# Performance work log

Hardware: AMD Instinct MI355X
Metric: run time of the kernel (lower is better)

Reference implementation:

```python
import jax, jax.numpy as jnp
import numpy as np

N_EMBED = 2048
N_HEAD = 16
HEAD_DIM = N_EMBED // N_HEAD
LN_EPS = 1e-5


def setup_inputs() -> dict:
    key = jax.random.key(0)
    ks = jax.random.split(key, 12)
    B, S, D = 4, 2048, N_EMBED
    s = 0.02
    inp = {
        "x": jax.random.normal(ks[0], (B, S, D), jnp.float32),
        "ln1_w": jnp.ones((D,), jnp.float32),
        "ln1_b": jnp.zeros((D,), jnp.float32),
        "Wqkv": jax.random.normal(ks[1], (3 * D, D), jnp.float32) * s,
        "bqkv": jnp.zeros((3 * D,), jnp.float32),
        "Wo": jax.random.normal(ks[2], (D, D), jnp.float32) * s,
        "bo": jnp.zeros((D,), jnp.float32),
        "ln2_w": jnp.ones((D,), jnp.float32),
        "ln2_b": jnp.zeros((D,), jnp.float32),
        "W1": jax.random.normal(ks[3], (4 * D, D), jnp.float32) * s,
        "b1": jnp.zeros((4 * D,), jnp.float32),
        "W2": jax.random.normal(ks[4], (D, 4 * D), jnp.float32) * s,
        "b2": jnp.zeros((D,), jnp.float32),
        # ALiBi slopes: 2^(-8*(h+1)/n_head)
        "slopes": jnp.asarray(2.0 ** (-8.0 * (np.arange(1, N_HEAD + 1)) / N_HEAD), jnp.float32),
    }
    return inp


def layer_norm(x, w, b):
    mu = jnp.mean(x, axis=-1, keepdims=True)
    var = jnp.mean(jnp.square(x - mu), axis=-1, keepdims=True)
    return (x - mu) * jax.lax.rsqrt(var + LN_EPS) * w + b


def attention(h, Wqkv, bqkv, Wo, bo, slopes):
    B, S, D = h.shape
    qkv = jnp.einsum("bsd,ed->bse", h, Wqkv) + bqkv  # [B,S,3D]
    q, k, v = jnp.split(qkv, 3, axis=-1)
    q = q.reshape(B, S, N_HEAD, HEAD_DIM).transpose(0, 2, 1, 3)
    k = k.reshape(B, S, N_HEAD, HEAD_DIM).transpose(0, 2, 1, 3)
    v = v.reshape(B, S, N_HEAD, HEAD_DIM).transpose(0, 2, 1, 3)
    scores = jnp.einsum("bhqd,bhkd->bhqk", q, k) / jnp.sqrt(jnp.float32(HEAD_DIM))
    pos = jnp.arange(S)
    rel = pos[None, :] - pos[:, None]  # j - i, <= 0 on causal part
    alibi = slopes[:, None, None] * rel[None, :, :].astype(jnp.float32)  # [H,S,S]
    causal = rel <= 0
    scores = jnp.where(causal[None, None], scores + alibi[None], -jnp.inf)
    attn = jax.nn.softmax(scores, axis=-1)
    out = jnp.einsum("bhqk,bhkd->bhqd", attn, v)
    out = out.transpose(0, 2, 1, 3).reshape(B, S, D)
    return jnp.einsum("bsd,ed->bse", out, Wo) + bo


def reference(x, ln1_w, ln1_b, Wqkv, bqkv, Wo, bo, ln2_w, ln2_b, W1, b1, W2, b2, slopes):
    # Pre-LN block; dropout in eval mode (identity)
    x = x + attention(layer_norm(x, ln1_w, ln1_b), Wqkv, bqkv, Wo, bo, slopes)
    h = layer_norm(x, ln2_w, ln2_b)
    h = jax.nn.gelu(jnp.einsum("bsd,fd->bsf", h, W1) + b1, approximate=False)
    x = x + jnp.einsum("bsf,df->bsd", h, W2) + b2
    return x
```

## Files before the change

### kernel.cpp

```cpp
#include <hip/hip_runtime.h>

typedef unsigned short ushort_t;
typedef __attribute__((ext_vector_type(8))) short short8;
typedef __attribute__((ext_vector_type(4))) float floatx4;
typedef __attribute__((ext_vector_type(4))) unsigned short ush4;

#define MFMA16x16x32(a, b, c) __builtin_amdgcn_mfma_f32_16x16x32_bf16(a, b, c, 0, 0, 0)

__device__ __forceinline__ float bf2f(ushort_t h) {
    unsigned int u = ((unsigned int)h) << 16;
    return __builtin_bit_cast(float, u);
}
__device__ __forceinline__ ushort_t f2bf(float f) {
    unsigned int u = __builtin_bit_cast(unsigned int, f);
    u += 0x7fffu + ((u >> 16) & 1u);
    return (ushort_t)(u >> 16);
}
__device__ __forceinline__ void gload_lds16(const ushort_t* g, ushort_t* l) {
    __builtin_amdgcn_global_load_lds(
        (const __attribute__((address_space(1))) unsigned int*)g,
        (__attribute__((address_space(3))) unsigned int*)l, 16, 0, 0);
}

__global__ __launch_bounds__(256) void conv_bf16(const float* __restrict__ in,
                                                 ushort_t* __restrict__ out, int n8) {
    int i = blockIdx.x * 256 + threadIdx.x;
    const int stride = gridDim.x * 256;
    for (; i < n8; i += stride) {
        const float* p = in + (size_t)i * 8;
        floatx4 a0 = *(const floatx4*)p;
        floatx4 a1 = *(const floatx4*)(p + 4);
        short8 o;
        o[0] = (short)f2bf(a0[0]); o[1] = (short)f2bf(a0[1]);
        o[2] = (short)f2bf(a0[2]); o[3] = (short)f2bf(a0[3]);
        o[4] = (short)f2bf(a1[0]); o[5] = (short)f2bf(a1[1]);
        o[6] = (short)f2bf(a1[2]); o[7] = (short)f2bf(a1[3]);
        *(short8*)(out + (size_t)i * 8) = o;
    }
}

template <int INF32>
__global__ __launch_bounds__(256) void ln_kernel(const void* __restrict__ in,
                                                 const ushort_t* __restrict__ w,
                                                 const ushort_t* __restrict__ b,
                                                 ushort_t* __restrict__ out) {
    const int row = blockIdx.x;
    const int tid = threadIdx.x;
    const size_t base = (size_t)row * 2048 + (size_t)tid * 8;
    float v[8];
    if (INF32) {
        const float* p = (const float*)in + base;
        floatx4 a0 = *(const floatx4*)p;
        floatx4 a1 = *(const floatx4*)(p + 4);
        v[0] = a0[0]; v[1] = a0[1]; v[2] = a0[2]; v[3] = a0[3];
        v[4] = a1[0]; v[5] = a1[1]; v[6] = a1[2]; v[7] = a1[3];
    } else {
        short8 hv = *(const short8*)((const ushort_t*)in + base);
        const ushort_t* hp = (const ushort_t*)&hv;
#pragma unroll
        for (int k = 0; k < 8; k++) v[k] = bf2f(hp[k]);
    }
    float s = 0.f, sq = 0.f;
#pragma unroll
    for (int k = 0; k < 8; k++) { s += v[k]; sq += v[k] * v[k]; }
#pragma unroll
    for (int m = 32; m; m >>= 1) { s += __shfl_xor(s, m); sq += __shfl_xor(sq, m); }
    __shared__ float red[8];
    const int wv = tid >> 6;
    if ((tid & 63) == 0) { red[wv] = s; red[4 + wv] = sq; }
    __syncthreads();
    s = red[0] + red[1] + red[2] + red[3];
    sq = red[4] + red[5] + red[6] + red[7];
    const float mu = s * (1.f / 2048.f);
    const float var = fmaxf(sq * (1.f / 2048.f) - mu * mu, 0.f);
    const float rs = rsqrtf(var + 1e-5f);
    short8 ov;
#pragma unroll
    for (int k = 0; k < 8; k++) {
        const int c = tid * 8 + k;
        float y = (v[k] - mu) * rs * bf2f(w[c]) + bf2f(b[c]);
        ov[k] = (short)f2bf(y);
    }
    *(short8*)(out + base) = ov;
}

template <int EPI>
__global__ __launch_bounds__(512, 2) void gemm256(const ushort_t* __restrict__ A,
                                                  const ushort_t* __restrict__ W,
                                                  const ushort_t* __restrict__ bias,
                                                  const void* __restrict__ res,
                                                  void* __restrict__ out,
                                                  int M, int N, int K) {
    __shared__ ushort_t smem[65536];
    const int tid = threadIdx.x;
    const int lane = tid & 63;
    const int wave = tid >> 6;
    const int la = lane & 15;
    const int qd = lane >> 4;
    const int wrow = (wave >> 2) * 128;
    const int wcol = (wave & 3) * 64;
    const int nbn = N >> 8;
    int bm, bn;
    {
        int wg = (int)blockIdx.x;
        const int cpx = (int)gridDim.x >> 3;
        wg = (wg & 7) * cpx + (wg >> 3);
        const int per = 8 * nbn;
        const int g = wg / per;
        const int rem = wg - g * per;
        bm = g * 8 + (rem & 7);
        bn = rem >> 3;
    }
    const int srow = tid >> 2;
    const int schunk = (tid & 3) ^ ((srow >> 1) & 3);
    const ushort_t* gA = A + (size_t)(bm * 256 + srow) * K + schunk * 8;
    const ushort_t* gB = W + (size_t)(bn * 256 + srow) * K + schunk * 8;
    const int wbase = (tid & ~63) * 8;
    const int kch = (qd ^ ((la >> 1) & 3)) * 8;

    floatx4 acc[8][4];
    const floatx4 z4 = {0.f, 0.f, 0.f, 0.f};
#pragma unroll
    for (int i = 0; i < 8; i++)
#pragma unroll
        for (int j = 0; j < 4; j++) acc[i][j] = z4;
    short8 a[8], b[4];

#define GBAR() __builtin_amdgcn_s_barrier()
#define GVM8() asm volatile("s_waitcnt vmcnt(8)")
#define STGA(koff, b_)                                                                  \
    do {                                                                                \
        gload_lds16(gA + (size_t)(koff), smem + (b_)*16384 + wbase);                    \
        gload_lds16(gA + (size_t)128 * K + (size_t)(koff),                              \
                    smem + (b_)*16384 + 4096 + wbase);                                  \
    } while (0)
#define STGB(koff, b_)                                                                  \
    do {                                                                                \
        gload_lds16(gB + (size_t)(koff), smem + (b_)*16384 + 8192 + wbase);             \
        gload_lds16(gB + (size_t)128 * K + (size_t)(koff),                              \
                    smem + (b_)*16384 + 12288 + wbase);                                 \
    } while (0)
#define LDAF(b_, mh)                                                                    \
    do {                                                                                \
        _Pragma("unroll") for (int mi = 0; mi < 4; mi++) {                              \
            a[(mh)*4 + mi] = *(const short8*)&smem[(b_)*16384 +                         \
                                          (wrow + (mh)*64 + mi * 16 + la) * 32 + kch];  \
        }                                                                               \
    } while (0)
#define LDBF(b_)                                                                        \
    do {                                                                                \
        _Pragma("unroll") for (int nj = 0; nj < 4; nj++) {                              \
            b[nj] = *(const short8*)&smem[(b_)*16384 + 8192 +                           \
                                          (wcol + nj * 16 + la) * 32 + kch];            \
        }                                                                               \
    } while (0)
#define MM32()                                                                          \
    do {                                                                                \
        _Pragma("unroll") for (int mi = 0; mi < 8; mi++)                                \
            _Pragma("unroll") for (int nj = 0; nj < 4; nj++) acc[mi][nj] =              \
                MFMA16x16x32(a[mi], b[nj], acc[mi][nj]);                                \
    } while (0)
#define KITER(u)                                                                        \
    do {                                                                                \
        GVM8();                                                                         \
        GBAR();                                                                         \
        const int pre_ = (t + (u) + 3 < NT) ? (t + (u) + 3) : (NT - 1);                 \
        const size_t ko_ = (size_t)pre_ * 32;                                           \
        STGA(ko_, ((u) + 3) & 3);                                                       \
        STGB(ko_, ((u) + 3) & 3);                                                       \
        LDAF((u), 0); LDBF((u)); LDAF((u), 1);                                          \
        __builtin_amdgcn_s_setprio(1); MM32(); __builtin_amdgcn_s_setprio(0);           \
    } while (0)

    const int NT = K >> 5;
    STGA(0, 0); STGB(0, 0);
    STGA(32, 1); STGB(32, 1);
    STGA(64, 2); STGB(64, 2);

    for (int t = 0; t < NT; t += 4) { KITER(0); KITER(1); KITER(2); KITER(3); }
    asm volatile("s_waitcnt vmcnt(0)");
    GBAR();
#undef GBAR
#undef GVM8
#undef STGA
#undef STGB
#undef LDAF
#undef LDBF
#undef MM32
#undef KITER

    if (EPI == 0) {
        ushort_t* q_out = (ushort_t*)out;
        if (bn < 16) {
            const float qs = (bn < 8) ? (0.08838834764831845f * 1.4426950408889634f) : 1.0f;
            ushort_t* dst = (bn < 8) ? q_out : (q_out + 16777216);
#pragma unroll
            for (int i = 0; i < 8; i++)
#pragma unroll
                for (int j = 0; j < 4; j++)
#pragma unroll
                    for (int r = 0; r < 4; r++) {
                        const int m = bm * 256 + wrow + i * 16 + qd * 4 + r;
                        const int n = bn * 256 + wcol + j * 16 + la;
                        dst[(size_t)m * 2048 + (n & 2047)] =
                            f2bf((acc[i][j][r] + bf2f(bias[n])) * qs);
                    }
        } else {
            ushort_t* v_out = q_out + 33554432;
#pragma unroll
            for (int i = 0; i < 8; i++)
#pragma unroll
                for (int j = 0; j < 4; j++) {
                    const int n = bn * 256 + wcol + j * 16 + la;
                    const int d = n - 4096;
                    const int m0 = bm * 256 + wrow + i * 16 + qd * 4;
                    const int bb = m0 >> 11, s = m0 & 2047;
                    const float bv = bf2f(bias[n]);
                    ush4 pk;
#pragma unroll
                    for (int r = 0; r < 4; r++) pk[r] = f2bf(acc[i][j][r] + bv);
                    *(ush4*)&v_out[((size_t)(bb * 2048 + d)) * 2048 + s] = pk;
                }
        }
    } else {
#pragma unroll
        for (int i = 0; i < 8; i++)
#pragma unroll
            for (int j = 0; j < 4; j++)
#pragma unroll
                for (int r = 0; r < 4; r++) {
                    const int m = bm * 256 + wrow + i * 16 + qd * 4 + r;
                    const int n = bn * 256 + wcol + j * 16 + la;
                    const size_t idx = (size_t)m * N + n;
                    float v = acc[i][j][r] + bf2f(bias[n]);
                    if (EPI == 1) {
                        v += ((const float*)res)[idx];
                        ((ushort_t*)out)[idx] = f2bf(v);
                    } else if (EPI == 2) {
                        v = 0.5f * v * (1.f + erff(v * 0.70710678118654752f));
                        ((ushort_t*)out)[idx] = f2bf(v);
                    } else {
                        v += bf2f(((const ushort_t*)res)[idx]);
                        ((float*)out)[idx] = v;
                    }
                }
    }
}

__global__ __launch_bounds__(256, 2) void attn_kernel(const ushort_t* __restrict__ qb,
                                                      const ushort_t* __restrict__ kb,
                                                      const ushort_t* __restrict__ vtb,
                                                      const float* __restrict__ slopes,
                                                      ushort_t* __restrict__ out) {
    __shared__ ushort_t Ks[16384];
    __shared__ ushort_t Vt[16384];
    __shared__ ushort_t Ps[4096];
    const int tid = threadIdx.x;
    const int lane = tid & 63;
    const int wave = tid >> 6;
    const int la = lane & 15;
    const int qd = lane >> 4;
    const int lid = (int)blockIdx.x;
    const int pair = (lid & 7) * 8 + (lid >> 8);
    const int h = pair & 15;
    const int b = pair >> 4;
    const int qt = 31 - ((lid >> 3) & 31);
    const float slope2 = slopes[h] * 1.4426950408889634f;

    const size_t qrow = (size_t)(b * 2048 + qt * 64 + wave * 16 + la);
    short8 qa[4];
#pragma unroll
    for (int ks = 0; ks < 4; ks++)
        qa[ks] = *(const short8*)&qb[qrow * 2048 + h * 128 + (ks * 4 + qd) * 8];

    const ushort_t* kbase = kb + ((size_t)b * 2048) * 2048 + h * 128;
    const ushort_t* vbase = vtb + ((size_t)(b * 2048 + h * 128)) * 2048;

    floatx4 accO[8];
    const floatx4 z4 = {0.f, 0.f, 0.f, 0.f};
#pragma unroll
    for (int dt = 0; dt < 8; dt++) accO[dt] = z4;
    float mst[4] = {-1e30f, -1e30f, -1e30f, -1e30f};
    float lst[4] = {0.f, 0.f, 0.f, 0.f};

#define AISSUE(kt_, buf_)                                                                   \
    do {                                                                                    \
        _Pragma("unroll") for (int p_ = 0; p_ < 4; p_++) {                                  \
            const int f_ = p_ * 256 + tid;                                                  \
            const int r_ = f_ >> 4;                                                         \
            const int cs_ = f_ & 15;                                                        \
            gload_lds16(kbase + (size_t)((kt_) * 64 + r_) * 2048 + (cs_ ^ (r_ & 15)) * 8,   \
                        Ks + (buf_) * 8192 + (size_t)(p_ * 256 + (tid & ~63)) * 8);         \
        }                                                                                   \
        _Pragma("unroll") for (int p_ = 0; p_ < 4; p_++) {                                  \
            const int f_ = p_ * 256 + tid;                                                  \
            const int d_ = f_ >> 3;                                                         \
            const int c_ = f_ & 7;                                                          \
            gload_lds16(vbase + (size_t)d_ * 2048 + (kt_) * 64 + (c_ ^ (d_ & 7)) * 8,       \
                        Vt + (buf_) * 8192 + (size_t)(p_ * 256 + (tid & ~63)) * 8);         \
        }                                                                                   \
    } while (0)
#define ABAR() __builtin_amdgcn_s_barrier()

    AISSUE(0, 0);
    for (int kt = 0; kt <= qt; kt++) {
        const int cur = kt & 1;
        if (kt < qt) {
            AISSUE(kt + 1, cur ^ 1);
            asm volatile("s_waitcnt vmcnt(8)");
        } else {
            asm volatile("s_waitcnt vmcnt(0)");
        }
        ABAR();
        const ushort_t* Kc = Ks + cur * 8192;
        const ushort_t* Vc = Vt + cur * 8192;

        floatx4 sc[4];
#pragma unroll
        for (int nt = 0; nt < 4; nt++) sc[nt] = z4;
#pragma unroll
        for (int nt = 0; nt < 4; nt++) {
#pragma unroll
            for (int ks = 0; ks < 4; ks++) {
                short8 kf = *(const short8*)&Kc[(nt * 16 + la) * 128 + ((ks * 4 + qd) ^ la) * 8];
                sc[nt] = MFMA16x16x32(qa[ks], kf, sc[nt]);
            }
        }

        const int knb = kt * 64;
        const bool diag = (kt == qt);
        ushort_t* Pw = Ps + wave * 1024;
        float acol[4];
#pragma unroll
        for (int nt = 0; nt < 4; nt++)
            acol[nt] = slope2 * (float)(knb + nt * 16 + la);
#pragma unroll
        for (int r = 0; r < 4; r++) {
            float rmax = -1e30f;
#pragma unroll
            for (int nt = 0; nt < 4; nt++) {
                float sval = sc[nt][r] + acol[nt];
                if (diag && (nt * 16 + la > wave * 16 + qd * 4 + r)) sval = -1e30f;
                sc[nt][r] = sval;
                rmax = fmaxf(rmax, sval);
            }
            rmax = fmaxf(rmax, __shfl_xor(rmax, 1));
            rmax = fmaxf(rmax, __shfl_xor(rmax, 2));
            rmax = fmaxf(rmax, __shfl_xor(rmax, 4));
            rmax = fmaxf(rmax, __shfl_xor(rmax, 8));
            const float mnew = fmaxf(mst[r], rmax);
            const int row = qd * 4 + r;
            float rsum = 0.f;
#pragma unroll
            for (int nt = 0; nt < 4; nt++) {
                const float pv = __builtin_amdgcn_exp2f(sc[nt][r] - mnew);
                rsum += pv;
                const int col = nt * 16 + la;
                Pw[row * 64 + ((col >> 3) ^ (row & 7)) * 8 + (col & 7)] = f2bf(pv);
            }
            rsum += __shfl_xor(rsum, 1);
            rsum += __shfl_xor(rsum, 2);
            rsum += __shfl_xor(rsum, 4);
            rsum += __shfl_xor(rsum, 8);
            const float alpha = __builtin_amdgcn_exp2f(mst[r] - mnew);
            mst[r] = mnew;
            lst[r] = lst[r] * alpha + rsum;
#pragma unroll
            for (int dt = 0; dt < 8; dt++) accO[dt][r] *= alpha;
        }

#pragma unroll
        for (int k2 = 0; k2 < 2; k2++) {
            short8 pa = *(const short8*)&Pw[la * 64 + ((k2 * 4 + qd) ^ (la & 7)) * 8];
#pragma unroll
            for (int dt = 0; dt < 8; dt++) {
                const int d = dt * 16 + la;
                short8 vf = *(const short8*)&Vc[d * 64 + ((k2 * 4 + qd) ^ (d & 7)) * 8];
                accO[dt] = MFMA16x16x32(pa, vf, accO[dt]);
            }
        }
        ABAR();
    }
#undef AISSUE
#undef ABAR

    const size_t orow0 = (size_t)b * 2048 + qt * 64 + wave * 16 + qd * 4;
#pragma unroll
    for (int r = 0; r < 4; r++) {
        const float inv = 1.f / lst[r];
#pragma unroll
        for (int dt = 0; dt < 8; dt++)
            out[(orow0 + r) * 2048 + h * 128 + dt * 16 + la] = f2bf(accO[dt][r] * inv);
    }
}

extern "C" void kernel_launch(void* const* d_in, const int* in_sizes, int n_in,
                              void* d_out, int out_size, void* d_ws, size_t ws_size,
                              hipStream_t stream) {
    (void)in_sizes; (void)n_in; (void)out_size; (void)ws_size;
    const float* x      = (const float*)d_in[0];
    const float* ln1w   = (const float*)d_in[1];
    const float* ln1b   = (const float*)d_in[2];
    const float* Wqkv   = (const float*)d_in[3];
    const float* bqkv   = (const float*)d_in[4];
    const float* Wo     = (const float*)d_in[5];
    const float* bo     = (const float*)d_in[6];
    const float* ln2w   = (const float*)d_in[7];
    const float* ln2b   = (const float*)d_in[8];
    const float* W1     = (const float*)d_in[9];
    const float* b1     = (const float*)d_in[10];
    const float* W2     = (const float*)d_in[11];
    const float* b2     = (const float*)d_in[12];
    const float* slopes = (const float*)d_in[13];
    float* outp = (float*)d_out;

    char* ws = (char*)d_ws;
    const size_t MB = 1ull << 20;
    ushort_t* wbuf  = (ushort_t*)(ws);
    ushort_t* sv    = (ushort_t*)(ws + 36 * MB);
    ushort_t* ln1w_c = sv;
    ushort_t* ln1b_c = sv + 2048;
    ushort_t* bqkv_c = sv + 4096;
    ushort_t* bo_c   = sv + 10240;
    ushort_t* ln2w_c = sv + 12288;
    ushort_t* ln2b_c = sv + 14336;
    ushort_t* b1_c   = sv + 16384;
    ushort_t* b2_c   = sv + 24576;
    ushort_t* h_buf    = (ushort_t*)(ws + 37 * MB);
    ushort_t* q_buf    = (ushort_t*)(ws + 69 * MB);
    ushort_t* k_buf    = (ushort_t*)(ws + 101 * MB);
    ushort_t* vt_buf   = (ushort_t*)(ws + 133 * MB);
    ushort_t* attn_buf = (ushort_t*)(ws + 165 * MB);
    ushort_t* act_buf  = q_buf;
    ushort_t* x2_buf   = (ushort_t*)(ws + 197 * MB);

    const int M = 8192;

    conv_bf16<<<8, 256, 0, stream>>>(ln1w, ln1w_c, 2048 / 8);
    conv_bf16<<<8, 256, 0, stream>>>(ln1b, ln1b_c, 2048 / 8);
    ln_kernel<1><<<M, 256, 0, stream>>>(x, ln1w_c, ln1b_c, h_buf);
    conv_bf16<<<2048, 256, 0, stream>>>(Wqkv, wbuf, (6144 * 2048) / 8);
    conv_bf16<<<8, 256, 0, stream>>>(bqkv, bqkv_c, 6144 / 8);
    gemm256<0><<<(M / 256) * (6144 / 256), 512, 0, stream>>>(
        h_buf, wbuf, bqkv_c, nullptr, q_buf, M, 6144, 2048);
    attn_kernel<<<2048, 256, 0, stream>>>(q_buf, k_buf, vt_buf, slopes, attn_buf);
    conv_bf16<<<1024, 256, 0, stream>>>(Wo, wbuf, (2048 * 2048) / 8);
    conv_bf16<<<8, 256, 0, stream>>>(bo, bo_c, 2048 / 8);
    gemm256<1><<<(M / 256) * (2048 / 256), 512, 0, stream>>>(
        attn_buf, wbuf, bo_c, x, x2_buf, M, 2048, 2048);
    conv_bf16<<<8, 256, 0, stream>>>(ln2w, ln2w_c, 2048 / 8);
    conv_bf16<<<8, 256, 0, stream>>>(ln2b, ln2b_c, 2048 / 8);
    ln_kernel<0><<<M, 256, 0, stream>>>(x2_buf, ln2w_c, ln2b_c, h_buf);
    conv_bf16<<<2048, 256, 0, stream>>>(W1, wbuf, (8192 * 2048) / 8);
    conv_bf16<<<8, 256, 0, stream>>>(b1, b1_c, 8192 / 8);
    gemm256<2><<<(M / 256) * (8192 / 256), 512, 0, stream>>>(
        h_buf, wbuf, b1_c, nullptr, act_buf, M, 8192, 2048);
    conv_bf16<<<2048, 256, 0, stream>>>(W2, wbuf, (2048 * 8192) / 8);
    conv_bf16<<<8, 256, 0, stream>>>(b2, b2_c, 2048 / 8);
    gemm256<3><<<(M / 256) * (2048 / 256), 512, 0, stream>>>(
        act_buf, wbuf, b2_c, x2_buf, outp, M, 2048, 8192);
}
```

Before: 1.270 ms.

## Double-buffer GEMM LDS fragments in registers to overlap loads with MFMA

The bf16 GEMM main loop now keeps two register sets of A/B fragments. It reads the next k-tile from LDS right after the barrier, then issues the global prefetch, then runs the MFMAs on the current tile. Base pointers per LDS stage are precomputed, and a sched_barrier keeps the compiler from moving the loads back into the MFMA block. The wait count and prologue change to match: an extra wait and barrier before the first fragment load. This hides LDS read latency behind matrix math, at the cost of roughly 64 more VGPRs for the second fragment set and a tighter synchronisation ordering.

```diff
diff --git a/kernel.cpp b/kernel.cpp
--- a/kernel.cpp
+++ b/kernel.cpp
@@ -117,6 +117,13 @@
     const ushort_t* gB = W + (size_t)(bn * 256 + srow) * K + schunk * 8;
     const int wbase = (tid & ~63) * 8;
     const int kch = (qd ^ ((la >> 1) & 3)) * 8;
+    const ushort_t* aB[4];
+    const ushort_t* bB[4];
+#pragma unroll
+    for (int q = 0; q < 4; q++) {
+        aB[q] = smem + q * 16384 + (wrow + la) * 32 + kch;
+        bB[q] = smem + q * 16384 + 8192 + (wcol + la) * 32 + kch;
+    }
 
     floatx4 acc[8][4];
     const floatx4 z4 = {0.f, 0.f, 0.f, 0.f};
@@ -124,10 +131,10 @@
     for (int i = 0; i < 8; i++)
 #pragma unroll
         for (int j = 0; j < 4; j++) acc[i][j] = z4;
-    short8 a[8], b[4];
+    short8 a[2][8], b[2][4];
 
 #define GBAR() __builtin_amdgcn_s_barrier()
-#define GVM8() asm volatile("s_waitcnt vmcnt(8)")
+#define GVM4() asm volatile("s_waitcnt vmcnt(4)")
 #define STGA(koff, b_)                                                                  \
     do {                                                                                \
         gload_lds16(gA + (size_t)(koff), smem + (b_)*16384 + wbase);                    \
@@ -140,52 +147,50 @@
         gload_lds16(gB + (size_t)128 * K + (size_t)(koff),                              \
                     smem + (b_)*16384 + 12288 + wbase);                                 \
     } while (0)
-#define LDAF(b_, mh)                                                                    \
+#define LDF(buf_, s_)                                                                   \
     do {                                                                                \
-        _Pragma("unroll") for (int mi = 0; mi < 4; mi++) {                              \
-            a[(mh)*4 + mi] = *(const short8*)&smem[(b_)*16384 +                         \
-                                          (wrow + (mh)*64 + mi * 16 + la) * 32 + kch];  \
-        }                                                                               \
-    } while (0)
-#define LDBF(b_)                                                                        \
-    do {                                                                                \
-        _Pragma("unroll") for (int nj = 0; nj < 4; nj++) {                              \
-            b[nj] = *(const short8*)&smem[(b_)*16384 + 8192 +                           \
-                                          (wcol + nj * 16 + la) * 32 + kch];            \
-        }                                                                               \
-    } while (0)
-#define MM32()                                                                          \
+        _Pragma("unroll") for (int mi = 0; mi < 4; mi++)                                \
+            a[s_][mi] = *(const short8*)(aB[buf_] + mi * 512);                          \
+        _Pragma("unroll") for (int nj = 0; nj < 4; nj++)                                \
+            b[s_][nj] = *(const short8*)(bB[buf_] + nj * 512);                          \
+        _Pragma("unroll") for (int mi = 0; mi < 4; mi++)                                \
+            a[s_][4 + mi] = *(const short8*)(aB[buf_] + 2048 + mi * 512);               \
+    } while (0)
+#define MM32(s_)                                                                        \
     do {                                                                                \
         _Pragma("unroll") for (int mi = 0; mi < 8; mi++)                                \
             _Pragma("unroll") for (int nj = 0; nj < 4; nj++) acc[mi][nj] =              \
-                MFMA16x16x32(a[mi], b[nj], acc[mi][nj]);                                \
+                MFMA16x16x32(a[s_][mi], b[s_][nj], acc[mi][nj]);                        \
     } while (0)
 #define KITER(u)                                                                        \
     do {                                                                                \
-        GVM8();                                                                         \
+        GVM4();                                                                         \
         GBAR();                                                                         \
+        LDF(((u) + 1) & 3, ((u) + 1) & 1);                                              \
         const int pre_ = (t + (u) + 3 < NT) ? (t + (u) + 3) : (NT - 1);                 \
         const size_t ko_ = (size_t)pre_ * 32;                                           \
         STGA(ko_, ((u) + 3) & 3);                                                       \
         STGB(ko_, ((u) + 3) & 3);                                                       \
-        LDAF((u), 0); LDBF((u)); LDAF((u), 1);                                          \
-        __builtin_amdgcn_s_setprio(1); MM32(); __builtin_amdgcn_s_setprio(0);           \
+        __builtin_amdgcn_sched_barrier(0);                                              \
+        __builtin_amdgcn_s_setprio(1); MM32((u) & 1); __builtin_amdgcn_s_setprio(0);    \
     } while (0)
 
     const int NT = K >> 5;
     STGA(0, 0); STGB(0, 0);
     STGA(32, 1); STGB(32, 1);
     STGA(64, 2); STGB(64, 2);
+    asm volatile("s_waitcnt vmcnt(8)");
+    GBAR();
+    LDF(0, 0);
 
     for (int t = 0; t < NT; t += 4) { KITER(0); KITER(1); KITER(2); KITER(3); }
     asm volatile("s_waitcnt vmcnt(0)");
     GBAR();
 #undef GBAR
-#undef GVM8
+#undef GVM4
 #undef STGA
 #undef STGB
-#undef LDAF
-#undef LDBF
+#undef LDF
 #undef MM32
 #undef KITER
 
```

New measurement: 1.422 ms. +11.9%, slower.
